# Kernel tuning notes

Hardware: AMD Instinct MI355X
Metric: run time of the kernel (lower is better)

## Reference

```python
import jax, jax.numpy as jnp
import numpy as np

B, S, K, H = 512, 128, 4, 128  # batch, seq_len, interest_num, hidden_size
ROUTING_TIMES = 3
EPS = 1e-9


def setup_inputs() -> dict:
    key = jax.random.key(0)
    k1, k2 = jax.random.split(key)
    item_eb = jax.random.normal(k1, (B, S, H), dtype=jnp.float32)
    mask = jnp.ones((B, S), dtype=jnp.float32)
    # learned bilinear map parameter (bilinear_type == 2)
    w = jax.random.normal(k2, (1, S, K * H, H), dtype=jnp.float32) * 0.02
    return {"item_eb": item_eb, "mask": mask, "w": w}


def _squash(cap):
    # cap: [B, K, 1, H]
    n = jnp.sum(cap * cap, axis=-1, keepdims=True)
    return (n / (1.0 + n) / jnp.sqrt(n + EPS)) * cap


def reference(item_eb, mask, w):
    # bilinear_type==2: sum(w[:, :S] * item_eb[:, :, None, :], axis=3)
    # expressed as an einsum to avoid the [B,S,K*H,H] intermediate
    item_eb_hat = jnp.einsum('bsh,sdh->bsd', item_eb, w[0])          # [B, S, K*H]
    item_eb_hat = item_eb_hat.reshape(B, S, K, H).transpose(0, 2, 1, 3)  # [B, K, S, H]
    hat_iter = jax.lax.stop_gradient(item_eb_hat)  # stop_grad=True

    atten_mask = jnp.broadcast_to(mask[:, None, :], (B, K, S))
    capsule_weight = jnp.zeros((B, K, S), dtype=item_eb.dtype)  # bilinear_type > 0

    interest_capsule = None
    for i in range(ROUTING_TIMES):
        # torch F.softmax with implicit dim on a 3D tensor -> dim=0 (legacy)
        sw = jax.nn.softmax(capsule_weight, axis=0)
        sw = jnp.where(atten_mask == 0, 0.0, sw)[:, :, None, :]  # [B, K, 1, S]
        src = hat_iter if i < 2 else item_eb_hat
        interest_capsule = _squash(jnp.matmul(sw, src))  # [B, K, 1, H]
        if i < 2:
            delta = jnp.matmul(hat_iter, interest_capsule.transpose(0, 1, 3, 2))  # [B,K,S,1]
            capsule_weight = capsule_weight + delta.reshape(B, K, S)

    return interest_capsule.reshape(B, K, H)
```

## Files before the change

### kernel.cpp

```cpp
#include <hip/hip_runtime.h>
#include <math.h>

#define BB 512
#define SS 128
#define KK 4
#define HH 128
#define DD 512

typedef __attribute__((ext_vector_type(8))) short bf16x8;
typedef __attribute__((ext_vector_type(4))) float f32x4;

__device__ __forceinline__ unsigned short f2bf(float f) {
  unsigned u = __float_as_uint(f);
  unsigned r = u + 0x7fffu + ((u >> 16) & 1u);
  return (unsigned short)(r >> 16);
}
__device__ __forceinline__ float bfhi(unsigned u) {
  return __uint_as_float(u & 0xffff0000u);
}
__device__ __forceinline__ float bflo(unsigned u) {
  return __uint_as_float(u << 16);
}

__global__ __launch_bounds__(256) void cvt_k(
    const float* __restrict__ in, unsigned short* __restrict__ out, int n4)
{
  int i = blockIdx.x * 256 + threadIdx.x;
  if (i < n4) {
    float4 v = ((const float4*)in)[i];
    ushort4 o;
    o.x = f2bf(v.x); o.y = f2bf(v.y); o.z = f2bf(v.z); o.w = f2bf(v.w);
    ((ushort4*)out)[i] = o;
  }
}

__global__ __launch_bounds__(256) void einsum_mfma(
    const unsigned short* __restrict__ A,
    const unsigned short* __restrict__ W,
    unsigned short* __restrict__ hat)
{
  __shared__ unsigned short Al[128 * 136];
  __shared__ unsigned short Wl[128 * 136];
  const int s  = blockIdx.z;
  const int b0 = blockIdx.x * 128;
  const int dt = blockIdx.y;
  const int d0 = dt * 128;
  const int t  = threadIdx.x;

  #pragma unroll
  for (int j = 0; j < 8; j++) {
    int f = t + 256 * j;
    int r = f >> 4, c = f & 15;
    const uint4* ga = (const uint4*)(A + ((size_t)(b0 + r) * SS + s) * HH);
    const uint4* gw = (const uint4*)(W + ((size_t)s * DD + d0 + r) * HH);
    *(uint4*)&Al[r * 136 + c * 8] = ga[c];
    *(uint4*)&Wl[r * 136 + c * 8] = gw[c];
  }
  __syncthreads();

  const int lane = t & 63, wv = t >> 6;
  const int qm = wv & 1, qn = wv >> 1;
  const int n16 = lane & 15, kq = lane >> 4;

  f32x4 acc[4][4] = {};
  #pragma unroll
  for (int kk = 0; kk < 4; kk++) {
    const int kbase = kk * 32 + kq * 8;
    bf16x8 af[4], bf[4];
    #pragma unroll
    for (int i = 0; i < 4; i++) {
      af[i] = *(const bf16x8*)&Al[(qm * 64 + i * 16 + n16) * 136 + kbase];
      bf[i] = *(const bf16x8*)&Wl[(qn * 64 + i * 16 + n16) * 136 + kbase];
    }
    #pragma unroll
    for (int i = 0; i < 4; i++)
      #pragma unroll
      for (int j = 0; j < 4; j++)
        acc[i][j] = __builtin_amdgcn_mfma_f32_16x16x32_bf16(af[i], bf[j], acc[i][j], 0, 0, 0);
  }

  #pragma unroll
  for (int i = 0; i < 4; i++) {
    #pragma unroll
    for (int reg = 0; reg < 4; reg++) {
      int b = b0 + qm * 64 + i * 16 + kq * 4 + reg;
      unsigned short* orow = hat + (((size_t)b * KK + dt) * SS + s) * HH;
      #pragma unroll
      for (int j = 0; j < 4; j++)
        orow[qn * 64 + j * 16 + n16] = f2bf(acc[i][j][reg]);
    }
  }
}

__global__ __launch_bounds__(256) void softmax_k(
    const float* __restrict__ cw, const float* __restrict__ mask,
    float* __restrict__ sw)
{
  __shared__ float rbuf[4];
  const int s = blockIdx.x, k = blockIdx.y, t = threadIdx.x;
  const size_t base = ((size_t)k * SS + s) * BB;
  float v0 = cw[base + t], v1 = cw[base + 256 + t];
  float m = fmaxf(v0, v1);
  #pragma unroll
  for (int o = 32; o; o >>= 1) m = fmaxf(m, __shfl_xor(m, o));
  if ((t & 63) == 0) rbuf[t >> 6] = m;
  __syncthreads();
  m = fmaxf(fmaxf(rbuf[0], rbuf[1]), fmaxf(rbuf[2], rbuf[3]));
  float e0 = expf(v0 - m), e1 = expf(v1 - m);
  float ssum = e0 + e1;
  #pragma unroll
  for (int o = 32; o; o >>= 1) ssum += __shfl_xor(ssum, o);
  __syncthreads();
  if ((t & 63) == 0) rbuf[t >> 6] = ssum;
  __syncthreads();
  float inv = 1.f / (rbuf[0] + rbuf[1] + rbuf[2] + rbuf[3]);
  float m0 = mask[(size_t)t * SS + s];
  float m1 = mask[(size_t)(t + 256) * SS + s];
  sw[base + t]       = (m0 == 0.f) ? 0.f : e0 * inv;
  sw[base + 256 + t] = (m1 == 0.f) ? 0.f : e1 * inv;
}

__global__ __launch_bounds__(256) void routing_k(
    const unsigned short* __restrict__ hat, const float* __restrict__ mask,
    const float* __restrict__ sw_in, float* __restrict__ cw,
    float* __restrict__ out, int mode)
{
  __shared__ float sw_l[128];
  __shared__ float4 red4[8][33];
  __shared__ float cq_l[128];
  const int b = blockIdx.x, k = blockIdx.y, t = threadIdx.x;

  if (t < 128) {
    if (mode == 0) {
      sw_l[t] = (mask[(size_t)b * SS + t] == 0.f) ? 0.f : (1.f / 512.f);
    } else {
      sw_l[t] = sw_in[((size_t)k * SS + t) * BB + b];
    }
  }
  __syncthreads();

  const unsigned short* hrow = hat + ((size_t)b * KK + k) * SS * HH;

  {
    const int h4 = t & 31, sg = t >> 5;
    const uint2* hp = (const uint2*)hrow;
    float4 a = make_float4(0.f, 0.f, 0.f, 0.f);
    #pragma unroll 4
    for (int i = 0; i < 16; i++) {
      int s = sg * 16 + i;
      uint2 v = hp[s * 32 + h4];
      float wv = sw_l[s];
      a.x = fmaf(wv, bflo(v.x), a.x);
      a.y = fmaf(wv, bfhi(v.x), a.y);
      a.z = fmaf(wv, bflo(v.y), a.z);
      a.w = fmaf(wv, bfhi(v.y), a.w);
    }
    red4[sg][h4] = a;
  }
  __syncthreads();

  if (t < 32) {
    float4 cap = red4[0][t];
    #pragma unroll
    for (int sg = 1; sg < 8; sg++) {
      float4 r = red4[sg][t];
      cap.x += r.x; cap.y += r.y; cap.z += r.z; cap.w += r.w;
    }
    float sq = cap.x * cap.x + cap.y * cap.y + cap.z * cap.z + cap.w * cap.w;
    #pragma unroll
    for (int o = 16; o; o >>= 1) sq += __shfl_xor(sq, o);
    const float n = sq;
    const float fac = n / (1.f + n) / sqrtf(n + 1e-9f);
    cap.x *= fac; cap.y *= fac; cap.z *= fac; cap.w *= fac;
    ((float4*)cq_l)[t] = cap;
    if (mode == 2)
      ((float4*)(out + ((size_t)b * KK + k) * HH))[t] = cap;
  }
  __syncthreads();

  if (mode < 2) {
    const int s = t >> 1, hh = t & 1;
    const uint4* hp16 = (const uint4*)hrow;
    float d = 0.f;
    #pragma unroll
    for (int j = 0; j < 8; j++) {
      uint4 v = hp16[s * 16 + hh * 8 + j];
      const float* cq = cq_l + hh * 64 + j * 8;
      d += bflo(v.x) * cq[0] + bfhi(v.x) * cq[1]
         + bflo(v.y) * cq[2] + bfhi(v.y) * cq[3]
         + bflo(v.z) * cq[4] + bfhi(v.z) * cq[5]
         + bflo(v.w) * cq[6] + bfhi(v.w) * cq[7];
    }
    d += __shfl_xor(d, 1);
    if (hh == 0) {
      float* p = cw + ((size_t)k * SS + s) * BB + b;
      if (mode == 0) *p = d; else *p += d;
    }
  }
}

extern "C" void kernel_launch(void* const* d_in, const int* in_sizes, int n_in,
                              void* d_out, int out_size, void* d_ws, size_t ws_size,
                              hipStream_t stream) {
  const float* item_eb = (const float*)d_in[0];
  const float* mask    = (const float*)d_in[1];
  const float* w       = (const float*)d_in[2];
  float* out = (float*)d_out;

  char* ws = (char*)d_ws;
  unsigned short* hat_bf  = (unsigned short*)ws;
  unsigned short* item_bf = (unsigned short*)(ws + 67108864);
  unsigned short* w_bf    = (unsigned short*)(ws + 83886080);
  float* cw  = (float*)(ws + 100663296);
  float* swb = (float*)(ws + 101711872);

  const int n4 = (BB * SS * HH) / 4;
  cvt_k<<<dim3(n4 / 256), 256, 0, stream>>>(item_eb, item_bf, n4);
  cvt_k<<<dim3(n4 / 256), 256, 0, stream>>>(w, w_bf, n4);

  einsum_mfma<<<dim3(4, 4, 128), 256, 0, stream>>>(item_bf, w_bf, hat_bf);

  routing_k<<<dim3(BB, KK), 256, 0, stream>>>(hat_bf, mask, nullptr, cw, out, 0);
  softmax_k<<<dim3(SS, KK), 256, 0, stream>>>(cw, mask, swb);
  routing_k<<<dim3(BB, KK), 256, 0, stream>>>(hat_bf, mask, swb, cw, out, 1);
  softmax_k<<<dim3(SS, KK), 256, 0, stream>>>(cw, mask, swb);
  routing_k<<<dim3(BB, KK), 256, 0, stream>>>(hat_bf, mask, swb, cw, out, 2);
}
```

Before: 198.4 us.

## Fuse fp32-to-bf16 conversion into einsum tile loads with swizzled LDS

Drops the two separate conversion kernels and has the einsum kernel load fp32 item and weight tiles directly, converting to bf16 as it writes shared memory. The K dimension is split into two 64-wide stages with an XOR-style swizzle in place of padding, and A and W are swapped in the MFMA operands so the output is written as ushort4 vectors instead of scalar stores. This removes the bf16 intermediate buffers and their extra HBM write and read plus two launches. In exchange the einsum kernel reads fp32 (twice the bytes per tile) and adds an extra barrier stage.

```diff
diff --git a/kernel.cpp b/kernel.cpp
--- a/kernel.cpp
+++ b/kernel.cpp
@@ -15,79 +15,80 @@
   unsigned r = u + 0x7fffu + ((u >> 16) & 1u);
   return (unsigned short)(r >> 16);
 }
-__device__ __forceinline__ float bfhi(unsigned u) {
-  return __uint_as_float(u & 0xffff0000u);
-}
-__device__ __forceinline__ float bflo(unsigned u) {
-  return __uint_as_float(u << 16);
-}
-
-__global__ __launch_bounds__(256) void cvt_k(
-    const float* __restrict__ in, unsigned short* __restrict__ out, int n4)
-{
-  int i = blockIdx.x * 256 + threadIdx.x;
-  if (i < n4) {
-    float4 v = ((const float4*)in)[i];
-    ushort4 o;
-    o.x = f2bf(v.x); o.y = f2bf(v.y); o.z = f2bf(v.z); o.w = f2bf(v.w);
-    ((ushort4*)out)[i] = o;
-  }
+__device__ __forceinline__ float bfhi(unsigned u) { return __uint_as_float(u & 0xffff0000u); }
+__device__ __forceinline__ float bflo(unsigned u) { return __uint_as_float(u << 16); }
+__device__ __forceinline__ unsigned pk2(float a, float b) {
+  return (unsigned)f2bf(a) | ((unsigned)f2bf(b) << 16);
 }
 
 __global__ __launch_bounds__(256) void einsum_mfma(
-    const unsigned short* __restrict__ A,
-    const unsigned short* __restrict__ W,
+    const float* __restrict__ A,
+    const float* __restrict__ W,
     unsigned short* __restrict__ hat)
 {
-  __shared__ unsigned short Al[128 * 136];
-  __shared__ unsigned short Wl[128 * 136];
+  __shared__ unsigned short Al[128 * 64];
+  __shared__ unsigned short Wl[128 * 64];
   const int s  = blockIdx.z;
   const int b0 = blockIdx.x * 128;
   const int dt = blockIdx.y;
   const int d0 = dt * 128;
   const int t  = threadIdx.x;
-
-  #pragma unroll
-  for (int j = 0; j < 8; j++) {
-    int f = t + 256 * j;
-    int r = f >> 4, c = f & 15;
-    const uint4* ga = (const uint4*)(A + ((size_t)(b0 + r) * SS + s) * HH);
-    const uint4* gw = (const uint4*)(W + ((size_t)s * DD + d0 + r) * HH);
-    *(uint4*)&Al[r * 136 + c * 8] = ga[c];
-    *(uint4*)&Wl[r * 136 + c * 8] = gw[c];
-  }
-  __syncthreads();
-
   const int lane = t & 63, wv = t >> 6;
   const int qm = wv & 1, qn = wv >> 1;
   const int n16 = lane & 15, kq = lane >> 4;
+  const int r = t >> 1, cq = t & 1;
 
   f32x4 acc[4][4] = {};
+
+  for (int ks = 0; ks < 128; ks += 64) {
+    const float* ga = A + ((size_t)(b0 + r) * SS + s) * HH + ks + cq * 32;
+    const float* gw = W + ((size_t)s * DD + d0 + r) * HH + ks + cq * 32;
+    #pragma unroll
+    for (int j = 0; j < 4; j++) {
+      float4 a0 = *(const float4*)(ga + 8 * j);
+      float4 a1 = *(const float4*)(ga + 8 * j + 4);
+      float4 w0 = *(const float4*)(gw + 8 * j);
+      float4 w1 = *(const float4*)(gw + 8 * j + 4);
+      const int goff = ((cq * 4 + j + r) & 7) * 8;
+      uint4 pa, pw;
+      pa.x = pk2(a0.x, a0.y); pa.y = pk2(a0.z, a0.w);
+      pa.z = pk2(a1.x, a1.y); pa.w = pk2(a1.z, a1.w);
+      pw.x = pk2(w0.x, w0.y); pw.y = pk2(w0.z, w0.w);
+      pw.z = pk2(w1.x, w1.y); pw.w = pk2(w1.z, w1.w);
+      *(uint4*)&Al[r * 64 + goff] = pa;
+      *(uint4*)&Wl[r * 64 + goff] = pw;
+    }
+    __syncthreads();
+    #pragma unroll
+    for (int kk = 0; kk < 2; kk++) {
+      bf16x8 af[4], bfr[4];
+      #pragma unroll
+      for (int i = 0; i < 4; i++) {
+        const int ra = qm * 64 + i * 16 + n16;
+        const int rb = qn * 64 + i * 16 + n16;
+        af[i]  = *(const bf16x8*)&Wl[ra * 64 + ((kk * 4 + kq + ra) & 7) * 8];
+        bfr[i] = *(const bf16x8*)&Al[rb * 64 + ((kk * 4 + kq + rb) & 7) * 8];
+      }
+      #pragma unroll
+      for (int i = 0; i < 4; i++)
+        #pragma unroll
+        for (int j = 0; j < 4; j++)
+          acc[i][j] = __builtin_amdgcn_mfma_f32_16x16x32_bf16(af[i], bfr[j], acc[i][j], 0, 0, 0);
+    }
+    __syncthreads();
+  }
+
   #pragma unroll
-  for (int kk = 0; kk < 4; kk++) {
-    const int kbase = kk * 32 + kq * 8;
-    bf16x8 af[4], bf[4];
+  for (int j = 0; j < 4; j++) {
+    const int b = b0 + qn * 64 + j * 16 + n16;
+    unsigned short* orow = hat + (((size_t)b * KK + dt) * SS + s) * HH;
     #pragma unroll
     for (int i = 0; i < 4; i++) {
-      af[i] = *(const bf16x8*)&Al[(qm * 64 + i * 16 + n16) * 136 + kbase];
-      bf[i] = *(const bf16x8*)&Wl[(qn * 64 + i * 16 + n16) * 136 + kbase];
-    }
-    #pragma unroll
-    for (int i = 0; i < 4; i++)
-      #pragma unroll
-      for (int j = 0; j < 4; j++)
-        acc[i][j] = __builtin_amdgcn_mfma_f32_16x16x32_bf16(af[i], bf[j], acc[i][j], 0, 0, 0);
-  }
-
-  #pragma unroll
-  for (int i = 0; i < 4; i++) {
-    #pragma unroll
-    for (int reg = 0; reg < 4; reg++) {
-      int b = b0 + qm * 64 + i * 16 + kq * 4 + reg;
-      unsigned short* orow = hat + (((size_t)b * KK + dt) * SS + s) * HH;
-      #pragma unroll
-      for (int j = 0; j < 4; j++)
-        orow[qn * 64 + j * 16 + n16] = f2bf(acc[i][j][reg]);
+      const int h = qm * 64 + i * 16 + kq * 4;
+      ushort4 o;
+      o.x = f2bf(acc[i][j][0]); o.y = f2bf(acc[i][j][1]);
+      o.z = f2bf(acc[i][j][2]); o.w = f2bf(acc[i][j][3]);
+      *(ushort4*)(orow + h) = o;
     }
   }
 }
@@ -208,17 +209,11 @@
   float* out = (float*)d_out;
 
   char* ws = (char*)d_ws;
-  unsigned short* hat_bf  = (unsigned short*)ws;
-  unsigned short* item_bf = (unsigned short*)(ws + 67108864);
-  unsigned short* w_bf    = (unsigned short*)(ws + 83886080);
-  float* cw  = (float*)(ws + 100663296);
-  float* swb = (float*)(ws + 101711872);
-
-  const int n4 = (BB * SS * HH) / 4;
-  cvt_k<<<dim3(n4 / 256), 256, 0, stream>>>(item_eb, item_bf, n4);
-  cvt_k<<<dim3(n4 / 256), 256, 0, stream>>>(w, w_bf, n4);
-
-  einsum_mfma<<<dim3(4, 4, 128), 256, 0, stream>>>(item_bf, w_bf, hat_bf);
+  unsigned short* hat_bf = (unsigned short*)ws;
+  float* cw  = (float*)(ws + 67108864);
+  float* swb = (float*)(ws + 68157440);
+
+  einsum_mfma<<<dim3(4, 4, 128), 256, 0, stream>>>(item_eb, w, hat_bf);
 
   routing_k<<<dim3(BB, KK), 256, 0, stream>>>(hat_bf, mask, nullptr, cw, out, 0);
   softmax_k<<<dim3(SS, KK), 256, 0, stream>>>(cw, mask, swb);
```

Result: slower. 209.1 us (+5.4%).
